# Optimization experiments

Hardware: AMD Instinct MI355X
Metric: run time of the kernel (lower is better)

Reference implementation:

```python
import jax, jax.numpy as jnp
import numpy as np

DIM = 1536
HEADS = 12
HD = DIM // HEADS           # 128
C = HD // 2                 # 64 rotary pairs per head
B = 1
F_, H_, W_ = 16, 16, 16
S = F_ * H_ * W_            # 4096
MAXPOS = 1024
EPS = 1e-6
SPLITS = (C - 2 * (C // 3), C // 3, C // 3)  # (22, 21, 21)


def setup_inputs() -> dict:
    key = jax.random.key(0)
    ks = jax.random.split(key, 8)
    std = 0.02
    x = jax.random.normal(ks[0], (B, S, DIM), jnp.float32)
    seq_lens = jnp.full((B,), S, dtype=jnp.int32)
    grid_sizes = jnp.tile(jnp.array([[F_, H_, W_]], jnp.int32), (B, 1))
    # rotary angle table: per split, theta_j = pos / 10000^(j/size)
    angs = []
    pos = jnp.arange(MAXPOS, dtype=jnp.float32)
    for sz in SPLITS:
        inv = 1.0 / (10000.0 ** (jnp.arange(sz, dtype=jnp.float32) / sz))
        angs.append(jnp.outer(pos, inv))
    freqs = jnp.concatenate(angs, axis=1)  # [MAXPOS, C]
    return {
        "x": x,
        "seq_lens": seq_lens,
        "grid_sizes": grid_sizes,
        "freqs": freqs,
        "wq": jax.random.normal(ks[1], (DIM, DIM), jnp.float32) * std,
        "bq": jnp.zeros((DIM,), jnp.float32),
        "wk": jax.random.normal(ks[2], (DIM, DIM), jnp.float32) * std,
        "bk": jnp.zeros((DIM,), jnp.float32),
        "wv": jax.random.normal(ks[3], (DIM, DIM), jnp.float32) * std,
        "bv": jnp.zeros((DIM,), jnp.float32),
        "wo": jax.random.normal(ks[4], (DIM, DIM), jnp.float32) * std,
        "bo": jnp.zeros((DIM,), jnp.float32),
        "gq": jnp.ones((DIM,), jnp.float32),
        "gk": jnp.ones((DIM,), jnp.float32),
    }


def _rms_norm(x, g):
    # x * rsqrt(mean(x^2) + eps) * g  (WanRMSNorm)
    var = jnp.mean(jnp.square(x), axis=-1, keepdims=True)
    return x * jax.lax.rsqrt(var + EPS) * g


def _rope(x, freqs, f, h, w):
    # x: [b, s, n, hd]; freqs: [MAXPOS, C] angles; grid (f,h,w), s = f*h*w
    fa = freqs[:f, : SPLITS[0]]
    ha = freqs[:h, SPLITS[0] : SPLITS[0] + SPLITS[1]]
    wa = freqs[:w, SPLITS[0] + SPLITS[1] :]
    ang = jnp.concatenate(
        [
            jnp.broadcast_to(fa[:, None, None, :], (f, h, w, SPLITS[0])),
            jnp.broadcast_to(ha[None, :, None, :], (f, h, w, SPLITS[1])),
            jnp.broadcast_to(wa[None, None, :, :], (f, h, w, SPLITS[2])),
        ],
        axis=-1,
    ).reshape(f * h * w, 1, C)  # [s, 1, C] broadcasts over heads
    cos, sin = jnp.cos(ang), jnp.sin(ang)
    xr = x[..., 0::2]  # real parts of complex pairs
    xi = x[..., 1::2]  # imag parts
    out_r = xr * cos - xi * sin
    out_i = xr * sin + xi * cos
    return jnp.stack([out_r, out_i], axis=-1).reshape(x.shape)


def reference(x, seq_lens, grid_sizes, freqs, wq, bq, wk, bk, wv, bv, wo, bo, gq, gk):
    b, s = x.shape[:2]
    q = _rms_norm(x @ wq.T + bq, gq).reshape(b, s, HEADS, HD)
    k = _rms_norm(x @ wk.T + bk, gk).reshape(b, s, HEADS, HD)
    v = (x @ wv.T + bv).reshape(b, s, HEADS, HD)
    # all samples share the same grid (static for jit)
    q = _rope(q, freqs, F_, H_, W_)
    k = _rope(k, freqs, F_, H_, W_)
    scale = 1.0 / np.sqrt(HD)
    scores = jnp.einsum("bqnd,bknd->bnqk", q, k) * scale  # [b, n, s, s]
    k_pos = jnp.arange(s)
    mask = k_pos[None, None, None, :] < seq_lens[:, None, None, None]
    scores = scores + jnp.where(mask, 0.0, -1e9)
    attn = jax.nn.softmax(scores, axis=-1)
    out = jnp.einsum("bnqk,bknd->bqnd", attn, v).reshape(b, s, DIM)
    return out @ wo.T + bo
```

## Files before the change

### kernel.cpp

```cpp
#include <hip/hip_runtime.h>
#include <hip/hip_bf16.h>

#define DIM   1536
#define HEADS 12
#define HD    128
#define SEQ   4096
#define QSCALE 0.08838834764831845f
#define LOG2E 1.44269504088896f

typedef __attribute__((ext_vector_type(8))) short short8;
typedef __attribute__((ext_vector_type(4))) float f32x4;
typedef __attribute__((ext_vector_type(16))) float f32x16;

__device__ __forceinline__ unsigned short f2bf(float f) {
    __hip_bfloat16 h = __float2bfloat16(f);
    return *reinterpret_cast<unsigned short*>(&h);
}
__device__ __forceinline__ float bf2f(unsigned short u) {
    return __uint_as_float(((unsigned int)u) << 16);
}
__device__ __forceinline__ void async_cp16(void* lds, const void* g) {
    __builtin_amdgcn_global_load_lds(
        (const __attribute__((address_space(1))) unsigned int*)g,
        (__attribute__((address_space(3))) unsigned int*)lds, 16, 0, 0);
}

__global__ __launch_bounds__(256) void convert_bf16(
    const float* __restrict__ src, __hip_bfloat16* __restrict__ dst, int n8)
{
    const int i = blockIdx.x * 256 + threadIdx.x;
    if (i >= n8) return;
    const float4 a = *reinterpret_cast<const float4*>(src + (size_t)i * 8);
    const float4 b = *reinterpret_cast<const float4*>(src + (size_t)i * 8 + 4);
    uint4 o;
    o.x = (unsigned int)f2bf(a.x) | ((unsigned int)f2bf(a.y) << 16);
    o.y = (unsigned int)f2bf(a.z) | ((unsigned int)f2bf(a.w) << 16);
    o.z = (unsigned int)f2bf(b.x) | ((unsigned int)f2bf(b.y) << 16);
    o.w = (unsigned int)f2bf(b.z) | ((unsigned int)f2bf(b.w) << 16);
    *reinterpret_cast<uint4*>(dst + (size_t)i * 8) = o;
}

__global__ __launch_bounds__(256) void gemm_qkv(
    const __hip_bfloat16* __restrict__ xb,
    const __hip_bfloat16* __restrict__ wqb, const float* __restrict__ bq,
    const __hip_bfloat16* __restrict__ wkb, const float* __restrict__ bk,
    const __hip_bfloat16* __restrict__ wvb, const float* __restrict__ bv,
    __hip_bfloat16* __restrict__ yq, __hip_bfloat16* __restrict__ yk,
    __hip_bfloat16* __restrict__ vrow)
{
    __shared__ __align__(16) short As[128][32];
    __shared__ __align__(16) short Bs[128][32];
    const int z  = blockIdx.z;
    const __hip_bfloat16* W = (z == 0) ? wqb : (z == 1) ? wkb : wvb;
    const float* bias = (z == 0) ? bq : (z == 1) ? bk : bv;
    __hip_bfloat16* outp = (z == 0) ? yq : (z == 1) ? yk : vrow;
    const int bm0 = blockIdx.x * 128;
    const int bn0 = blockIdx.y * 128;
    const int tid  = threadIdx.x;
    const int lane = tid & 63;
    const int wid  = tid >> 6;
    const int wm = (wid >> 1) * 64;
    const int wn = (wid & 1)  * 64;
    const int fr = lane & 15;
    const int fc = (lane >> 4) * 8;
    const int srow = tid >> 2;
    const int scol = (tid & 3) * 8;

    f32x4 acc[4][4] = {};

    for (int kt = 0; kt < DIM; kt += 32) {
        #pragma unroll
        for (int i = 0; i < 2; i++) {
            async_cp16(&As[i * 64 + ((tid >> 6) << 4)][0],
                       xb + (size_t)(bm0 + i * 64 + srow) * DIM + kt + scol);
            async_cp16(&Bs[i * 64 + ((tid >> 6) << 4)][0],
                       W + (size_t)(bn0 + i * 64 + srow) * DIM + kt + scol);
        }
        __syncthreads();
        short8 af[4], bf8[4];
        #pragma unroll
        for (int m = 0; m < 4; m++) af[m]  = *reinterpret_cast<const short8*>(&As[wm + m * 16 + fr][fc]);
        #pragma unroll
        for (int n = 0; n < 4; n++) bf8[n] = *reinterpret_cast<const short8*>(&Bs[wn + n * 16 + fr][fc]);
        #pragma unroll
        for (int m = 0; m < 4; m++)
            #pragma unroll
            for (int n = 0; n < 4; n++)
                acc[m][n] = __builtin_amdgcn_mfma_f32_16x16x32_bf16(af[m], bf8[n], acc[m][n], 0, 0, 0);
        __syncthreads();
    }

    const int crow0 = bm0 + wm + (lane >> 4) * 4;
    const int ccol0 = bn0 + wn + fr;
    #pragma unroll
    for (int n = 0; n < 4; n++) {
        const int col = ccol0 + n * 16;
        const float bb = bias[col];
        #pragma unroll
        for (int m = 0; m < 4; m++)
            #pragma unroll
            for (int r = 0; r < 4; r++)
                outp[(size_t)(crow0 + m * 16 + r) * DIM + col] =
                    __float2bfloat16(acc[m][n][r] + bb);
    }
}

__global__ __launch_bounds__(256) void rmsnorm_rope(
    __hip_bfloat16* __restrict__ yq, __hip_bfloat16* __restrict__ yk,
    const float* __restrict__ gq, const float* __restrict__ gk,
    const float* __restrict__ freqs)
{
    const int s = blockIdx.x;
    const int z = blockIdx.y;
    __hip_bfloat16* y = z ? yk : yq;
    const float* g = z ? gk : gq;
    const int t = threadIdx.x;

    float xr[3], xi[3];
    float ss = 0.f;
    #pragma unroll
    for (int i = 0; i < 3; i++) {
        const int p = t + i * 256;
        const unsigned int uu = *reinterpret_cast<const unsigned int*>(&y[(size_t)s * DIM + 2 * p]);
        xr[i] = bf2f((unsigned short)(uu & 0xffffu));
        xi[i] = bf2f((unsigned short)(uu >> 16));
        ss += xr[i] * xr[i] + xi[i] * xi[i];
    }
    #pragma unroll
    for (int m = 1; m < 64; m <<= 1) ss += __shfl_xor(ss, m, 64);
    __shared__ float red[4];
    if ((t & 63) == 0) red[t >> 6] = ss;
    __syncthreads();
    const float sum = red[0] + red[1] + red[2] + red[3];
    const float rs = rsqrtf(sum * (1.0f / DIM) + 1e-6f);
    const int f = s >> 8, hh = (s >> 4) & 15, ww = s & 15;
    const float osc = z ? 1.0f : QSCALE;
    #pragma unroll
    for (int i = 0; i < 3; i++) {
        const int p = t + i * 256;
        const int cc = p & 63;
        const int pos = (cc < 22) ? f : (cc < 43) ? hh : ww;
        const float ang = freqs[pos * 64 + cc];
        float sn, cs;
        sincosf(ang, &sn, &cs);
        const float a = xr[i] * rs * g[2 * p];
        const float b = xi[i] * rs * g[2 * p + 1];
        const unsigned int pk = (unsigned int)f2bf((a * cs - b * sn) * osc)
                              | ((unsigned int)f2bf((a * sn + b * cs) * osc) << 16);
        *reinterpret_cast<unsigned int*>(&y[(size_t)s * DIM + 2 * p]) = pk;
    }
}

__global__ __launch_bounds__(256) void transpose_v(
    const __hip_bfloat16* __restrict__ vrow,
    __hip_bfloat16* __restrict__ vT)
{
    __shared__ __align__(16) short tile[64][72];
    const int s0 = blockIdx.x * 64;
    const int c0 = blockIdx.y * 64;
    const int t = threadIdx.x;
    #pragma unroll
    for (int i = 0; i < 2; i++) {
        const int ch = t + i * 256;
        const int r = ch >> 3, cc = (ch & 7) * 8;
        *reinterpret_cast<int4*>(&tile[r][cc]) =
            *reinterpret_cast<const int4*>(&vrow[(size_t)(s0 + r) * DIM + c0 + cc]);
    }
    __syncthreads();
    #pragma unroll
    for (int i = 0; i < 2; i++) {
        const int ch = t + i * 256;
        const int c = ch & 63, sc = (ch >> 6) * 8;
        unsigned int w0 = (unsigned short)tile[sc + 0][c] | ((unsigned int)(unsigned short)tile[sc + 1][c] << 16);
        unsigned int w1 = (unsigned short)tile[sc + 2][c] | ((unsigned int)(unsigned short)tile[sc + 3][c] << 16);
        unsigned int w2 = (unsigned short)tile[sc + 4][c] | ((unsigned int)(unsigned short)tile[sc + 5][c] << 16);
        unsigned int w3 = (unsigned short)tile[sc + 6][c] | ((unsigned int)(unsigned short)tile[sc + 7][c] << 16);
        int4 val;
        val.x = (int)w0; val.y = (int)w1; val.z = (int)w2; val.w = (int)w3;
        *reinterpret_cast<int4*>(&vT[(size_t)(c0 + c) * SEQ + s0 + sc]) = val;
    }
}

__global__ __launch_bounds__(256, 2) void flash_attn(
    const __hip_bfloat16* __restrict__ qb,
    const __hip_bfloat16* __restrict__ kb,
    const __hip_bfloat16* __restrict__ vT,
    const int* __restrict__ seq_lens,
    __hip_bfloat16* __restrict__ attno)
{
    __shared__ __align__(16) short Ks[2][64][128];
    __shared__ __align__(16) short Vs[2][128][64];
    const int qt = blockIdx.x;
    const int h  = blockIdx.y;
    const int tid = threadIdx.x;
    const int lane = tid & 63;
    const int w = tid >> 6;
    const int q5 = lane & 31;
    const int hi = lane >> 5;
    const int seqlen = seq_lens[0];
    const int swz = (lane & 7) << 4;

    short8 qf[8];
    const int qrow = qt * 128 + w * 32 + q5;
    #pragma unroll
    for (int s = 0; s < 8; s++)
        qf[s] = *reinterpret_cast<const short8*>(&qb[(size_t)qrow * DIM + h * HD + s * 16 + hi * 8]);

    f32x16 oacc[4] = {};
    float m = -1e30f, l = 0.f;

    const int kROW = w * 4 + (lane >> 4);
    const int kCOL = ((lane & 15) ^ (kROW & 7)) * 8;
    const int vROW = w * 8 + (lane >> 3);
    const int vCOL = (((lane & 7) ^ (vROW & 7))) * 8;

    #pragma unroll
    for (int i = 0; i < 4; i++) {
        async_cp16(&Ks[0][i * 16 + w * 4][0],
                   kb + (size_t)(i * 16 + kROW) * DIM + h * HD + kCOL);
        async_cp16(&Vs[0][i * 32 + w * 8][0],
                   vT + ((size_t)h * HD + i * 32 + vROW) * SEQ + vCOL);
    }
    __syncthreads();

    for (int t = 0; t < SEQ / 64; t++) {
        const int cur = t & 1;
        const int kbase = t * 64;
        if (t + 1 < SEQ / 64) {
            const int nb = kbase + 64;
            #pragma unroll
            for (int i = 0; i < 4; i++) {
                async_cp16(&Ks[cur ^ 1][i * 16 + w * 4][0],
                           kb + (size_t)(nb + i * 16 + kROW) * DIM + h * HD + kCOL);
                async_cp16(&Vs[cur ^ 1][i * 32 + w * 8][0],
                           vT + ((size_t)h * HD + i * 32 + vROW) * SEQ + nb + vCOL);
            }
        }
        const char* Kp = (const char*)&Ks[cur][0][0];
        const char* Vp = (const char*)&Vs[cur][0][0];

        f32x16 sacc[2] = {};
        __builtin_amdgcn_s_setprio(1);
        #pragma unroll
        for (int s = 0; s < 8; s++) {
            #pragma unroll
            for (int kbk = 0; kbk < 2; kbk++) {
                short8 kf = *reinterpret_cast<const short8*>(
                    Kp + (kbk * 32 + q5) * 256 + ((s * 32 + hi * 16) ^ swz));
                sacc[kbk] = __builtin_amdgcn_mfma_f32_32x32x16_bf16(kf, qf[s], sacc[kbk], 0, 0, 0);
            }
        }
        __builtin_amdgcn_s_setprio(0);

        float tmax = -1e30f;
        if (kbase + 64 <= seqlen) {
            #pragma unroll
            for (int kbk = 0; kbk < 2; kbk++)
                #pragma unroll
                for (int r = 0; r < 16; r++) tmax = fmaxf(tmax, sacc[kbk][r]);
        } else {
            #pragma unroll
            for (int kbk = 0; kbk < 2; kbk++) {
                #pragma unroll
                for (int r = 0; r < 16; r++) {
                    const int key = kbase + kbk * 32 + (r & 3) + 8 * (r >> 2) + 4 * hi;
                    const float sv = (key < seqlen) ? sacc[kbk][r] : -1e30f;
                    sacc[kbk][r] = sv;
                    tmax = fmaxf(tmax, sv);
                }
            }
        }
        tmax = fmaxf(tmax, __shfl_xor(tmax, 32, 64));

        if (!__all(tmax <= m + 8.0f)) {
            const float mn = fmaxf(m, tmax);
            const float alpha = exp2f((m - mn) * LOG2E);
            m = mn;
            l *= alpha;
            #pragma unroll
            for (int cb = 0; cb < 4; cb++)
                #pragma unroll
                for (int r = 0; r < 16; r++) oacc[cb][r] *= alpha;
        }

        float ps = 0.f;
        #pragma unroll
        for (int kbk = 0; kbk < 2; kbk++) {
            #pragma unroll
            for (int r = 0; r < 16; r++) {
                const float p = exp2f((sacc[kbk][r] - m) * LOG2E);
                sacc[kbk][r] = p;
                ps += p;
            }
        }
        ps += __shfl_xor(ps, 32, 64);
        l += ps;

        unsigned int W[2][4][2];
        #pragma unroll
        for (int kbk = 0; kbk < 2; kbk++)
            #pragma unroll
            for (int tq = 0; tq < 4; tq++) {
                W[kbk][tq][0] = (unsigned int)f2bf(sacc[kbk][4 * tq + 0])
                              | ((unsigned int)f2bf(sacc[kbk][4 * tq + 1]) << 16);
                W[kbk][tq][1] = (unsigned int)f2bf(sacc[kbk][4 * tq + 2])
                              | ((unsigned int)f2bf(sacc[kbk][4 * tq + 3]) << 16);
            }

        #pragma unroll
        for (int ks = 0; ks < 4; ks++) {
            const int kbk = ks >> 1;
            const int te = (ks & 1) * 2, to = te + 1;
            const int a0 = (int)W[kbk][te][0], a1 = (int)W[kbk][te][1];
            const int b0 = (int)W[kbk][to][0], b1 = (int)W[kbk][to][1];
            const int xa0 = __shfl_xor(a0, 32, 64);
            const int xa1 = __shfl_xor(a1, 32, 64);
            const int xb0 = __shfl_xor(b0, 32, 64);
            const int xb1 = __shfl_xor(b1, 32, 64);
            int4 pwv;
            pwv.x = hi ? xb0 : a0;
            pwv.y = hi ? xb1 : a1;
            pwv.z = hi ? b0  : xa0;
            pwv.w = hi ? b1  : xa1;
            const short8 pf = __builtin_bit_cast(short8, pwv);
            __builtin_amdgcn_s_setprio(1);
            #pragma unroll
            for (int cb = 0; cb < 4; cb++) {
                short8 vf = *reinterpret_cast<const short8*>(
                    Vp + (cb * 32 + q5) * 128 + ((ks * 32 + hi * 16) ^ swz));
                oacc[cb] = __builtin_amdgcn_mfma_f32_32x32x16_bf16(vf, pf, oacc[cb], 0, 0, 0);
            }
            __builtin_amdgcn_s_setprio(0);
        }
        __syncthreads();
    }

    const float inv_l = 1.f / l;
    const size_t obase = (size_t)qrow * DIM + h * HD;
    #pragma unroll
    for (int cb = 0; cb < 4; cb++) {
        #pragma unroll
        for (int tq = 0; tq < 4; tq++) {
            uint2 pko;
            pko.x = (unsigned int)f2bf(oacc[cb][4 * tq + 0] * inv_l)
                  | ((unsigned int)f2bf(oacc[cb][4 * tq + 1] * inv_l) << 16);
            pko.y = (unsigned int)f2bf(oacc[cb][4 * tq + 2] * inv_l)
                  | ((unsigned int)f2bf(oacc[cb][4 * tq + 3] * inv_l) << 16);
            *reinterpret_cast<uint2*>(&attno[obase + cb * 32 + 8 * tq + 4 * hi]) = pko;
        }
    }
}

__global__ __launch_bounds__(256) void gemm_out(
    const __hip_bfloat16* __restrict__ A,
    const __hip_bfloat16* __restrict__ W,
    const float* __restrict__ bias,
    float* __restrict__ outp)
{
    __shared__ __align__(16) short As[128][32];
    __shared__ __align__(16) short Bs[128][32];
    const int bm0 = blockIdx.x * 128;
    const int bn0 = blockIdx.y * 128;
    const int tid = threadIdx.x;
    const int lane = tid & 63;
    const int wid = tid >> 6;
    const int wm = (wid >> 1) * 64;
    const int wn = (wid & 1) * 64;
    const int fr = lane & 15;
    const int fc = (lane >> 4) * 8;
    const int srow = tid >> 2;
    const int scol = (tid & 3) * 8;

    f32x4 acc[4][4] = {};

    for (int kt = 0; kt < DIM; kt += 32) {
        #pragma unroll
        for (int i = 0; i < 2; i++) {
            async_cp16(&As[i * 64 + ((tid >> 6) << 4)][0],
                       A + (size_t)(bm0 + i * 64 + srow) * DIM + kt + scol);
            async_cp16(&Bs[i * 64 + ((tid >> 6) << 4)][0],
                       W + (size_t)(bn0 + i * 64 + srow) * DIM + kt + scol);
        }
        __syncthreads();
        short8 af[4], bf8[4];
        #pragma unroll
        for (int m = 0; m < 4; m++) af[m]  = *reinterpret_cast<const short8*>(&As[wm + m * 16 + fr][fc]);
        #pragma unroll
        for (int n = 0; n < 4; n++) bf8[n] = *reinterpret_cast<const short8*>(&Bs[wn + n * 16 + fr][fc]);
        #pragma unroll
        for (int m = 0; m < 4; m++)
            #pragma unroll
            for (int n = 0; n < 4; n++)
                acc[m][n] = __builtin_amdgcn_mfma_f32_16x16x32_bf16(af[m], bf8[n], acc[m][n], 0, 0, 0);
        __syncthreads();
    }

    const int crow0 = bm0 + wm + (lane >> 4) * 4;
    const int ccol0 = bn0 + wn + fr;
    #pragma unroll
    for (int n = 0; n < 4; n++) {
        const int col = ccol0 + n * 16;
        const float bb = bias[col];
        #pragma unroll
        for (int m = 0; m < 4; m++)
            #pragma unroll
            for (int r = 0; r < 4; r++)
                outp[(size_t)(crow0 + m * 16 + r) * DIM + col] = acc[m][n][r] + bb;
    }
}

extern "C" void kernel_launch(void* const* d_in, const int* in_sizes, int n_in,
                              void* d_out, int out_size, void* d_ws, size_t ws_size,
                              hipStream_t stream)
{
    const float* x        = (const float*)d_in[0];
    const int*   seq_lens = (const int*)d_in[1];
    const float* freqs    = (const float*)d_in[3];
    const float* wq = (const float*)d_in[4];
    const float* bq = (const float*)d_in[5];
    const float* wk = (const float*)d_in[6];
    const float* bk = (const float*)d_in[7];
    const float* wv = (const float*)d_in[8];
    const float* bv = (const float*)d_in[9];
    const float* wo = (const float*)d_in[10];
    const float* bo = (const float*)d_in[11];
    const float* gq = (const float*)d_in[12];
    const float* gk = (const float*)d_in[13];
    float* out = (float*)d_out;

    char* ws = (char*)d_ws;
    __hip_bfloat16* yq    = (__hip_bfloat16*)(ws);
    __hip_bfloat16* yk    = (__hip_bfloat16*)(ws + 12582912);
    __hip_bfloat16* vrow  = (__hip_bfloat16*)(ws + 25165824);
    __hip_bfloat16* vT    = (__hip_bfloat16*)(ws + 37748736);
    __hip_bfloat16* attno = (__hip_bfloat16*)(ws + 25165824);
    __hip_bfloat16* xb    = (__hip_bfloat16*)(ws + 37748736);
    __hip_bfloat16* wob   = (__hip_bfloat16*)(ws);
    __hip_bfloat16* wqb   = (__hip_bfloat16*)d_out;
    __hip_bfloat16* wkb   = wqb + 2359296;
    __hip_bfloat16* wvb   = wkb + 2359296;

    dim3 blk(256);
    convert_bf16<<<dim3(3072), blk, 0, stream>>>(x,  xb,  786432);
    convert_bf16<<<dim3(1152), blk, 0, stream>>>(wq, wqb, 294912);
    convert_bf16<<<dim3(1152), blk, 0, stream>>>(wk, wkb, 294912);
    convert_bf16<<<dim3(1152), blk, 0, stream>>>(wv, wvb, 294912);
    gemm_qkv    <<<dim3(32, 12, 3), blk, 0, stream>>>(xb, wqb, bq, wkb, bk, wvb, bv, yq, yk, vrow);
    rmsnorm_rope<<<dim3(4096, 2),   blk, 0, stream>>>(yq, yk, gq, gk, freqs);
    transpose_v <<<dim3(64, 24),    blk, 0, stream>>>(vrow, vT);
    flash_attn  <<<dim3(32, 12),    blk, 0, stream>>>(yq, yk, vT, seq_lens, attno);
    convert_bf16<<<dim3(1152), blk, 0, stream>>>(wo, wob, 294912);
    gemm_out    <<<dim3(32, 12),    blk, 0, stream>>>(attno, wob, bo, out);
}
```

Measured before the change: 358.7 us.

## Shrink flash attention blocks to two waves and single-buffer V tile

Flash attention now launches 128-thread blocks covering 64 query rows, doubling the grid to 768 blocks. On 256 CUs the old 384-block grid left many CUs idle, so this spreads work more evenly. The V tile in LDS is single-buffered and loaded at the start of each iteration, with a barrier before the PV MFMAs. K stays double-buffered with a new load pattern. Less LDS per block allows more resident blocks, but V load latency is now exposed within each iteration, an extra barrier is added, and each K/V tile is read by twice as many blocks.

After: 356.9 us. No clear change (-0.5%).

```diff
diff --git a/kernel.cpp b/kernel.cpp
--- a/kernel.cpp
+++ b/kernel.cpp
@@ -181,7 +181,7 @@
     }
 }
 
-__global__ __launch_bounds__(256, 2) void flash_attn(
+__global__ __launch_bounds__(128, 2) void flash_attn(
     const __hip_bfloat16* __restrict__ qb,
     const __hip_bfloat16* __restrict__ kb,
     const __hip_bfloat16* __restrict__ vT,
@@ -189,7 +189,7 @@
     __hip_bfloat16* __restrict__ attno)
 {
     __shared__ __align__(16) short Ks[2][64][128];
-    __shared__ __align__(16) short Vs[2][128][64];
+    __shared__ __align__(16) short Vs[128][64];
     const int qt = blockIdx.x;
     const int h  = blockIdx.y;
     const int tid = threadIdx.x;
@@ -201,7 +201,7 @@
     const int swz = (lane & 7) << 4;
 
     short8 qf[8];
-    const int qrow = qt * 128 + w * 32 + q5;
+    const int qrow = qt * 64 + w * 32 + q5;
     #pragma unroll
     for (int s = 0; s < 8; s++)
         qf[s] = *reinterpret_cast<const short8*>(&qb[(size_t)qrow * DIM + h * HD + s * 16 + hi * 8]);
@@ -209,35 +209,33 @@
     f32x16 oacc[4] = {};
     float m = -1e30f, l = 0.f;
 
-    const int kROW = w * 4 + (lane >> 4);
-    const int kCOL = ((lane & 15) ^ (kROW & 7)) * 8;
-    const int vROW = w * 8 + (lane >> 3);
-    const int vCOL = (((lane & 7) ^ (vROW & 7))) * 8;
-
-    #pragma unroll
-    for (int i = 0; i < 4; i++) {
-        async_cp16(&Ks[0][i * 16 + w * 4][0],
-                   kb + (size_t)(i * 16 + kROW) * DIM + h * HD + kCOL);
-        async_cp16(&Vs[0][i * 32 + w * 8][0],
-                   vT + ((size_t)h * HD + i * 32 + vROW) * SEQ + vCOL);
-    }
-    __syncthreads();
+    const int kROW0 = w * 4 + (lane >> 4);
+    const int kCOL  = ((lane & 15) ^ kROW0) * 8;
+    const int vROW0 = w * 8 + (lane >> 3);
+    const int vCOL  = ((lane & 7) ^ (vROW0 & 7)) * 8;
+
+    #pragma unroll
+    for (int i = 0; i < 8; i++)
+        async_cp16(&Ks[0][i * 8 + w * 4][0],
+                   kb + (size_t)(i * 8 + kROW0) * DIM + h * HD + kCOL);
 
     for (int t = 0; t < SEQ / 64; t++) {
-        const int cur = t & 1;
         const int kbase = t * 64;
+        __syncthreads();
+
+        #pragma unroll
+        for (int i = 0; i < 8; i++)
+            async_cp16(&Vs[i * 16 + vROW0][0],
+                       vT + ((size_t)h * HD + i * 16 + vROW0) * SEQ + kbase + vCOL);
         if (t + 1 < SEQ / 64) {
             const int nb = kbase + 64;
             #pragma unroll
-            for (int i = 0; i < 4; i++) {
-                async_cp16(&Ks[cur ^ 1][i * 16 + w * 4][0],
-                           kb + (size_t)(nb + i * 16 + kROW) * DIM + h * HD + kCOL);
-                async_cp16(&Vs[cur ^ 1][i * 32 + w * 8][0],
-                           vT + ((size_t)h * HD + i * 32 + vROW) * SEQ + nb + vCOL);
-            }
-        }
-        const char* Kp = (const char*)&Ks[cur][0][0];
-        const char* Vp = (const char*)&Vs[cur][0][0];
+            for (int i = 0; i < 8; i++)
+                async_cp16(&Ks[(t + 1) & 1][i * 8 + w * 4][0],
+                           kb + (size_t)(nb + i * 8 + kROW0) * DIM + h * HD + kCOL);
+        }
+
+        const char* Kp = (const char*)&Ks[t & 1][0][0];
 
         f32x16 sacc[2] = {};
         __builtin_amdgcn_s_setprio(1);
@@ -307,6 +305,9 @@
                               | ((unsigned int)f2bf(sacc[kbk][4 * tq + 3]) << 16);
             }
 
+        __syncthreads();
+
+        const char* Vp = (const char*)&Vs[0][0];
         #pragma unroll
         for (int ks = 0; ks < 4; ks++) {
             const int kbk = ks >> 1;
@@ -332,7 +333,6 @@
             }
             __builtin_amdgcn_s_setprio(0);
         }
-        __syncthreads();
     }
 
     const float inv_l = 1.f / l;
@@ -448,7 +448,7 @@
     gemm_qkv    <<<dim3(32, 12, 3), blk, 0, stream>>>(xb, wqb, bq, wkb, bk, wvb, bv, yq, yk, vrow);
     rmsnorm_rope<<<dim3(4096, 2),   blk, 0, stream>>>(yq, yk, gq, gk, freqs);
     transpose_v <<<dim3(64, 24),    blk, 0, stream>>>(vrow, vT);
-    flash_attn  <<<dim3(32, 12),    blk, 0, stream>>>(yq, yk, vT, seq_lens, attno);
+    flash_attn  <<<dim3(64, 12),    dim3(128), 0, stream>>>(yq, yk, vT, seq_lens, attno);
     convert_bf16<<<dim3(1152), blk, 0, stream>>>(wo, wob, 294912);
     gemm_out    <<<dim3(32, 12),    blk, 0, stream>>>(attno, wob, bo, out);
 }
```

## Software-pipeline flash attention: overlap PV of previous tile with QK of current

Applied to the files above, without the earlier changes.

Restructures the attention loop so each iteration issues the QK MFMAs for tile t, then the PV MFMAs for tile t-1 using probabilities kept in registers, then does the softmax for tile t. A prologue handles the first tile and an epilogue handles the last PV. V gets a third LDS buffer because three tiles are now live at once. The aim is to hide softmax exp and max work and the shuffles behind matrix-core work. The cost is more LDS per block, which may limit occupancy, and more live registers.

Result: faster. 330.1 us (-8.0%).

```diff
diff --git a/kernel.cpp b/kernel.cpp
--- a/kernel.cpp
+++ b/kernel.cpp
@@ -189,7 +189,7 @@
     __hip_bfloat16* __restrict__ attno)
 {
     __shared__ __align__(16) short Ks[2][64][128];
-    __shared__ __align__(16) short Vs[2][128][64];
+    __shared__ __align__(16) short Vs[3][128][64];
     const int qt = blockIdx.x;
     const int h  = blockIdx.y;
     const int tid = threadIdx.x;
@@ -199,6 +199,7 @@
     const int hi = lane >> 5;
     const int seqlen = seq_lens[0];
     const int swz = (lane & 7) << 4;
+    const int NT = SEQ / 64;
 
     short8 qf[8];
     const int qrow = qt * 128 + w * 32 + q5;
@@ -208,6 +209,7 @@
 
     f32x16 oacc[4] = {};
     float m = -1e30f, l = 0.f;
+    unsigned int Wp[2][4][2];
 
     const int kROW = w * 4 + (lane >> 4);
     const int kCOL = ((lane & 15) ^ (kROW & 7)) * 8;
@@ -218,39 +220,123 @@
     for (int i = 0; i < 4; i++) {
         async_cp16(&Ks[0][i * 16 + w * 4][0],
                    kb + (size_t)(i * 16 + kROW) * DIM + h * HD + kCOL);
-        async_cp16(&Vs[0][i * 32 + w * 8][0],
+        async_cp16(&Vs[0][i * 32 + vROW][0],
                    vT + ((size_t)h * HD + i * 32 + vROW) * SEQ + vCOL);
     }
     __syncthreads();
 
-    for (int t = 0; t < SEQ / 64; t++) {
-        const int cur = t & 1;
-        const int kbase = t * 64;
-        if (t + 1 < SEQ / 64) {
-            const int nb = kbase + 64;
-            #pragma unroll
-            for (int i = 0; i < 4; i++) {
-                async_cp16(&Ks[cur ^ 1][i * 16 + w * 4][0],
-                           kb + (size_t)(nb + i * 16 + kROW) * DIM + h * HD + kCOL);
-                async_cp16(&Vs[cur ^ 1][i * 32 + w * 8][0],
-                           vT + ((size_t)h * HD + i * 32 + vROW) * SEQ + nb + vCOL);
-            }
-        }
-        const char* Kp = (const char*)&Ks[cur][0][0];
-        const char* Vp = (const char*)&Vs[cur][0][0];
-
+    {
+        #pragma unroll
+        for (int i = 0; i < 4; i++) {
+            async_cp16(&Ks[1][i * 16 + w * 4][0],
+                       kb + (size_t)(64 + i * 16 + kROW) * DIM + h * HD + kCOL);
+            async_cp16(&Vs[1][i * 32 + vROW][0],
+                       vT + ((size_t)h * HD + i * 32 + vROW) * SEQ + 64 + vCOL);
+        }
+        const char* Kp = (const char*)&Ks[0][0][0];
         f32x16 sacc[2] = {};
         __builtin_amdgcn_s_setprio(1);
         #pragma unroll
-        for (int s = 0; s < 8; s++) {
+        for (int s = 0; s < 8; s++)
             #pragma unroll
             for (int kbk = 0; kbk < 2; kbk++) {
                 short8 kf = *reinterpret_cast<const short8*>(
                     Kp + (kbk * 32 + q5) * 256 + ((s * 32 + hi * 16) ^ swz));
                 sacc[kbk] = __builtin_amdgcn_mfma_f32_32x32x16_bf16(kf, qf[s], sacc[kbk], 0, 0, 0);
             }
-        }
         __builtin_amdgcn_s_setprio(0);
+        float tmax = -1e30f;
+        #pragma unroll
+        for (int kbk = 0; kbk < 2; kbk++)
+            #pragma unroll
+            for (int r = 0; r < 16; r++) {
+                const int key = kbk * 32 + (r & 3) + 8 * (r >> 2) + 4 * hi;
+                const float sv = (key < seqlen) ? sacc[kbk][r] : -1e30f;
+                sacc[kbk][r] = sv;
+                tmax = fmaxf(tmax, sv);
+            }
+        tmax = fmaxf(tmax, __shfl_xor(tmax, 32, 64));
+        const float mn = fmaxf(m, tmax);
+        m = mn;
+        float ps = 0.f;
+        #pragma unroll
+        for (int kbk = 0; kbk < 2; kbk++)
+            #pragma unroll
+            for (int r = 0; r < 16; r++) {
+                const float p = exp2f((sacc[kbk][r] - m) * LOG2E);
+                sacc[kbk][r] = p;
+                ps += p;
+            }
+        ps += __shfl_xor(ps, 32, 64);
+        l = ps;
+        #pragma unroll
+        for (int kbk = 0; kbk < 2; kbk++)
+            #pragma unroll
+            for (int tq = 0; tq < 4; tq++) {
+                Wp[kbk][tq][0] = (unsigned int)f2bf(sacc[kbk][4 * tq + 0])
+                               | ((unsigned int)f2bf(sacc[kbk][4 * tq + 1]) << 16);
+                Wp[kbk][tq][1] = (unsigned int)f2bf(sacc[kbk][4 * tq + 2])
+                               | ((unsigned int)f2bf(sacc[kbk][4 * tq + 3]) << 16);
+            }
+    }
+
+    int vprev = 0, vnext = 2;
+    for (int t = 1; t < NT; t++) {
+        const int kbase = t * 64;
+        __syncthreads();
+
+        if (t + 1 < NT) {
+            const int nb = kbase + 64;
+            #pragma unroll
+            for (int i = 0; i < 4; i++) {
+                async_cp16(&Ks[(t + 1) & 1][i * 16 + w * 4][0],
+                           kb + (size_t)(nb + i * 16 + kROW) * DIM + h * HD + kCOL);
+                async_cp16(&Vs[vnext][i * 32 + vROW][0],
+                           vT + ((size_t)h * HD + i * 32 + vROW) * SEQ + nb + vCOL);
+            }
+        }
+
+        const char* Kp = (const char*)&Ks[t & 1][0][0];
+        f32x16 sacc[2] = {};
+        __builtin_amdgcn_s_setprio(1);
+        #pragma unroll
+        for (int s = 0; s < 8; s++)
+            #pragma unroll
+            for (int kbk = 0; kbk < 2; kbk++) {
+                short8 kf = *reinterpret_cast<const short8*>(
+                    Kp + (kbk * 32 + q5) * 256 + ((s * 32 + hi * 16) ^ swz));
+                sacc[kbk] = __builtin_amdgcn_mfma_f32_32x32x16_bf16(kf, qf[s], sacc[kbk], 0, 0, 0);
+            }
+        __builtin_amdgcn_s_setprio(0);
+
+        {
+            const char* Vp = (const char*)&Vs[vprev][0][0];
+            #pragma unroll
+            for (int ks = 0; ks < 4; ks++) {
+                const int kbk = ks >> 1;
+                const int te = (ks & 1) * 2, to = te + 1;
+                const int a0 = (int)Wp[kbk][te][0], a1 = (int)Wp[kbk][te][1];
+                const int b0 = (int)Wp[kbk][to][0], b1 = (int)Wp[kbk][to][1];
+                const int xa0 = __shfl_xor(a0, 32, 64);
+                const int xa1 = __shfl_xor(a1, 32, 64);
+                const int xb0 = __shfl_xor(b0, 32, 64);
+                const int xb1 = __shfl_xor(b1, 32, 64);
+                int4 pwv;
+                pwv.x = hi ? xb0 : a0;
+                pwv.y = hi ? xb1 : a1;
+                pwv.z = hi ? b0  : xa0;
+                pwv.w = hi ? b1  : xa1;
+                const short8 pf = __builtin_bit_cast(short8, pwv);
+                __builtin_amdgcn_s_setprio(1);
+                #pragma unroll
+                for (int cb = 0; cb < 4; cb++) {
+                    short8 vf = *reinterpret_cast<const short8*>(
+                        Vp + (cb * 32 + q5) * 128 + ((ks * 32 + hi * 16) ^ swz));
+                    oacc[cb] = __builtin_amdgcn_mfma_f32_32x32x16_bf16(vf, pf, oacc[cb], 0, 0, 0);
+                }
+                __builtin_amdgcn_s_setprio(0);
+            }
+        }
 
         float tmax = -1e30f;
         if (kbase + 64 <= seqlen) {
@@ -260,7 +346,7 @@
                 for (int r = 0; r < 16; r++) tmax = fmaxf(tmax, sacc[kbk][r]);
         } else {
             #pragma unroll
-            for (int kbk = 0; kbk < 2; kbk++) {
+            for (int kbk = 0; kbk < 2; kbk++)
                 #pragma unroll
                 for (int r = 0; r < 16; r++) {
                     const int key = kbase + kbk * 32 + (r & 3) + 8 * (r >> 2) + 4 * hi;
@@ -268,10 +354,8 @@
                     sacc[kbk][r] = sv;
                     tmax = fmaxf(tmax, sv);
                 }
-            }
         }
         tmax = fmaxf(tmax, __shfl_xor(tmax, 32, 64));
-
         if (!__all(tmax <= m + 8.0f)) {
             const float mn = fmaxf(m, tmax);
             const float alpha = exp2f((m - mn) * LOG2E);
@@ -282,37 +366,39 @@
                 #pragma unroll
                 for (int r = 0; r < 16; r++) oacc[cb][r] *= alpha;
         }
-
         float ps = 0.f;
         #pragma unroll
-        for (int kbk = 0; kbk < 2; kbk++) {
+        for (int kbk = 0; kbk < 2; kbk++)
             #pragma unroll
             for (int r = 0; r < 16; r++) {
                 const float p = exp2f((sacc[kbk][r] - m) * LOG2E);
                 sacc[kbk][r] = p;
                 ps += p;
             }
-        }
         ps += __shfl_xor(ps, 32, 64);
         l += ps;
-
-        unsigned int W[2][4][2];
         #pragma unroll
         for (int kbk = 0; kbk < 2; kbk++)
             #pragma unroll
             for (int tq = 0; tq < 4; tq++) {
-                W[kbk][tq][0] = (unsigned int)f2bf(sacc[kbk][4 * tq + 0])
-                              | ((unsigned int)f2bf(sacc[kbk][4 * tq + 1]) << 16);
-                W[kbk][tq][1] = (unsigned int)f2bf(sacc[kbk][4 * tq + 2])
-                              | ((unsigned int)f2bf(sacc[kbk][4 * tq + 3]) << 16);
-            }
-
+                Wp[kbk][tq][0] = (unsigned int)f2bf(sacc[kbk][4 * tq + 0])
+                               | ((unsigned int)f2bf(sacc[kbk][4 * tq + 1]) << 16);
+                Wp[kbk][tq][1] = (unsigned int)f2bf(sacc[kbk][4 * tq + 2])
+                               | ((unsigned int)f2bf(sacc[kbk][4 * tq + 3]) << 16);
+            }
+
+        vprev = (vprev == 2) ? 0 : vprev + 1;
+        vnext = (vnext == 2) ? 0 : vnext + 1;
+    }
+
+    {
+        const char* Vp = (const char*)&Vs[vprev][0][0];
         #pragma unroll
         for (int ks = 0; ks < 4; ks++) {
             const int kbk = ks >> 1;
             const int te = (ks & 1) * 2, to = te + 1;
-            const int a0 = (int)W[kbk][te][0], a1 = (int)W[kbk][te][1];
-            const int b0 = (int)W[kbk][to][0], b1 = (int)W[kbk][to][1];
+            const int a0 = (int)Wp[kbk][te][0], a1 = (int)Wp[kbk][te][1];
+            const int b0 = (int)Wp[kbk][to][0], b1 = (int)Wp[kbk][to][1];
             const int xa0 = __shfl_xor(a0, 32, 64);
             const int xa1 = __shfl_xor(a1, 32, 64);
             const int xb0 = __shfl_xor(b0, 32, 64);
@@ -323,16 +409,13 @@
             pwv.z = hi ? b0  : xa0;
             pwv.w = hi ? b1  : xa1;
             const short8 pf = __builtin_bit_cast(short8, pwv);
-            __builtin_amdgcn_s_setprio(1);
             #pragma unroll
             for (int cb = 0; cb < 4; cb++) {
                 short8 vf = *reinterpret_cast<const short8*>(
                     Vp + (cb * 32 + q5) * 128 + ((ks * 32 + hi * 16) ^ swz));
                 oacc[cb] = __builtin_amdgcn_mfma_f32_32x32x16_bf16(vf, pf, oacc[cb], 0, 0, 0);
             }
-            __builtin_amdgcn_s_setprio(0);
-        }
-        __syncthreads();
+        }
     }
 
     const float inv_l = 1.f / l;
```
